# Kernel tuning notes

Hardware: AMD Instinct MI355X
Metric: run time of the kernel (lower is better)

Reference implementation:

```python
import jax, jax.numpy as jnp
import numpy as np

B, C_IN, L = 16, 64, 1024
HID, OUT, ORDER = 1024, 512, 4
EPS = 1e-5


def setup_inputs() -> dict:
    key = jax.random.key(0)
    ks = jax.random.split(key, 4)
    return {
        "x": jax.random.normal(ks[0], (B, C_IN, L), jnp.float32),
        "W_in": jax.random.normal(ks[1], (C_IN, HID), jnp.float32) / np.sqrt(C_IN).astype(np.float32),
        "b_in": jnp.zeros((HID,), jnp.float32),
        "coeffs1": jax.random.normal(ks[2], (HID, HID, ORDER), jnp.float32) * 0.01,
        "bias1": jnp.zeros((HID,), jnp.float32),
        "g1": jnp.ones((HID,), jnp.float32),
        "beta1": jnp.zeros((HID,), jnp.float32),
        "coeffs2": jax.random.normal(ks[3], (OUT, HID, ORDER), jnp.float32) * 0.01,
        "bias2": jnp.zeros((OUT,), jnp.float32),
        "g2": jnp.ones((OUT,), jnp.float32),
        "beta2": jnp.zeros((OUT,), jnp.float32),
    }


def _taylor_kan(x, coeffs, bias):
    # x: (B, L, C_in); coeffs: (out, C_in, order); y[b,l,o] = sum_i sum_c x^i * coeffs[o,c,i]
    # Expressed as order-wise GEMMs with a running power -- no (B,out,L,C) expand.
    order = coeffs.shape[-1]
    y = jnp.zeros(x.shape[:2] + (coeffs.shape[0],), x.dtype)
    xp = jnp.ones_like(x)  # x**0 (matches torch 0**0 == 1)
    for i in range(order):
        y = y + jnp.einsum('blc,oc->blo', xp, coeffs[:, :, i])
        if i + 1 < order:
            xp = xp * x
    return y + bias


def _layernorm(x, g, b):
    mu = jnp.mean(x, -1, keepdims=True)
    var = jnp.mean((x - mu) ** 2, -1, keepdims=True)
    return (x - mu) * jax.lax.rsqrt(var + EPS) * g + b


def reference(x, W_in, b_in, coeffs1, bias1, g1, beta1, coeffs2, bias2, g2, beta2):
    # x: (B, C_in, L) -> project channels to hidden: (B, L, HID)
    h = jnp.einsum('bcl,ch->blh', x, W_in) + b_in
    h = _taylor_kan(h, coeffs1, bias1)            # (B, L, HID)
    h = jax.nn.gelu(_layernorm(h, g1, beta1), approximate=False)
    h = _taylor_kan(h, coeffs2, bias2)            # (B, L, OUT)
    h = _layernorm(h, g2, beta2)
    return jnp.mean(h, axis=1)                    # adaptive avg pool over L -> (B, OUT)
```

## Files before the change

kernel.cpp:

```cpp
#include <hip/hip_runtime.h>
#include <math.h>

#define Bsz  16
#define CIN  64
#define LEN  1024
#define HIDN 1024
#define OUTN 512
#define MTOT (Bsz*LEN)
#define KTOT (3*HIDN)
#define KT1  (2*HIDN + CIN)
#define LCHUNKS 32
#define LROWS   (LEN/LCHUNKS)

typedef __attribute__((ext_vector_type(8))) short bf16x8;
typedef __attribute__((ext_vector_type(16))) float f32x16;

__device__ __forceinline__ unsigned short f2bf(float x) {
    union { float f; unsigned int u; } v; v.f = x;
    unsigned int r = v.u + 0x7fff + ((v.u >> 16) & 1);
    return (unsigned short)(r >> 16);
}
__device__ __forceinline__ float bf2f(unsigned short u) {
    union { unsigned int u; float f; } v; v.u = ((unsigned int)u) << 16;
    return v.f;
}
__device__ __forceinline__ void gload_lds16(const void* g, void* l) {
    __builtin_amdgcn_global_load_lds((const __attribute__((address_space(1))) void*)g,
                                     (__attribute__((address_space(3))) void*)l, 16, 0, 0);
}

__global__ __launch_bounds__(256) void prep_all(const float* __restrict__ coeffs1,
                                                const float* __restrict__ bias1,
                                                const float* __restrict__ coeffs2,
                                                const float* __restrict__ bias2,
                                                const float* __restrict__ x,
                                                const float* __restrict__ Win,
                                                unsigned short* __restrict__ W1T,
                                                float* __restrict__ b1e,
                                                unsigned short* __restrict__ W2T,
                                                float* __restrict__ b2e,
                                                unsigned short* __restrict__ xT,
                                                unsigned short* __restrict__ WinT) {
    __shared__ float sm[64 * 65];
    int bid = blockIdx.x, t = threadIdx.x;
    if (bid < 1024) {
        int o = bid;
        float s = 0.f;
        unsigned short* wrow = W1T + (size_t)o * KT1;
        for (int c = t; c < HIDN; c += 256) {
            float4 v = *(const float4*)(coeffs1 + ((size_t)o * HIDN + c) * 4);
            s += v.x;
            wrow[c]        = f2bf(v.z);
            wrow[HIDN + c] = f2bf(v.w);
        }
        for (int off = 32; off > 0; off >>= 1) s += __shfl_down(s, off, 64);
        if ((t & 63) == 0) sm[t >> 6] = s;
        __syncthreads();
        if (t == 0) b1e[o] = bias1[o] + sm[0] + sm[1] + sm[2] + sm[3];
    } else if (bid < 1536) {
        int o = bid - 1024;
        float s = 0.f;
        unsigned short* wrow = W2T + (size_t)o * KTOT;
        for (int c = t; c < HIDN; c += 256) {
            float4 v = *(const float4*)(coeffs2 + ((size_t)o * HIDN + c) * 4);
            s += v.x;
            wrow[c]            = f2bf(v.y);
            wrow[HIDN + c]     = f2bf(v.z);
            wrow[2 * HIDN + c] = f2bf(v.w);
        }
        for (int off = 32; off > 0; off >>= 1) s += __shfl_down(s, off, 64);
        if ((t & 63) == 0) sm[t >> 6] = s;
        __syncthreads();
        if (t == 0) b2e[o] = bias2[o] + sm[0] + sm[1] + sm[2] + sm[3];
    } else {
        const float* src; unsigned short* dstbase; size_t src_rstride;
        int c0;
        if (bid < 1792) {
            int tile = bid - 1536; int b = tile >> 4; c0 = (tile & 15) * 64;
            src = x + (size_t)b * CIN * LEN;  src_rstride = LEN;
            dstbase = xT + ((size_t)b * LEN + c0) * CIN;
        } else {
            int tile = bid - 1792; c0 = tile * 64;
            src = Win; src_rstride = HIDN;
            dstbase = WinT + (size_t)c0 * CIN;
        }
#pragma unroll
        for (int it = 0; it < 4; it++) {
            int idx = t + it * 256;
            int c = idx >> 4, q = idx & 15;
            float4 v = *(const float4*)(src + (size_t)c * src_rstride + c0 + q * 4);
            sm[c * 65 + q * 4 + 0] = v.x;
            sm[c * 65 + q * 4 + 1] = v.y;
            sm[c * 65 + q * 4 + 2] = v.z;
            sm[c * 65 + q * 4 + 3] = v.w;
        }
        __syncthreads();
        int ll = t >> 2, cg = (t & 3) * 16;
        unsigned short* dst = dstbase + (size_t)ll * CIN + cg;
#pragma unroll
        for (int j = 0; j < 4; j++) {
            int c = cg + j * 4;
            ushort4 w = { f2bf(sm[(c + 0) * 65 + ll]), f2bf(sm[(c + 1) * 65 + ll]),
                          f2bf(sm[(c + 2) * 65 + ll]), f2bf(sm[(c + 3) * 65 + ll]) };
            *(ushort4*)(dst + j * 4) = w;
        }
    }
}

__global__ __launch_bounds__(256) void wc1_kernel(const float* __restrict__ coeffs1,
                                                  const unsigned short* __restrict__ WinT,
                                                  const float* __restrict__ bin,
                                                  unsigned short* __restrict__ W1T,
                                                  float* __restrict__ b1e) {
    __shared__ float c1s[HIDN];
    __shared__ float part[4][64];
    __shared__ float pbred[4];
    int o = blockIdx.x, t = threadIdx.x, lane = t & 63, wave = t >> 6;
    for (int c = t; c < HIDN; c += 256)
        c1s[c] = coeffs1[((size_t)o * HIDN + c) * 4 + 1];
    __syncthreads();
    float acc = 0.f;
    int cbase = wave * 256;
    for (int c = cbase; c < cbase + 256; c++)
        acc += bf2f(WinT[c * CIN + lane]) * c1s[c];
    part[wave][lane] = acc;
    float pb = 0.f;
    for (int c = t; c < HIDN; c += 256) pb += bin[c] * c1s[c];
    for (int off = 32; off > 0; off >>= 1) pb += __shfl_down(pb, off, 64);
    if (lane == 0) pbred[wave] = pb;
    __syncthreads();
    if (t < 64) {
        float v = part[0][t] + part[1][t] + part[2][t] + part[3][t];
        W1T[(size_t)o * KT1 + 2 * HIDN + t] = f2bf(v);
    }
    if (t == 0) b1e[o] += pbred[0] + pbred[1] + pbred[2] + pbred[3];
}

__global__ __launch_bounds__(256) void proj_mfma(const unsigned short* __restrict__ xT,
                                                 const unsigned short* __restrict__ WinT,
                                                 const float* __restrict__ bin,
                                                 unsigned short* __restrict__ A1) {
    __shared__ unsigned short smem[2 * 128 * 64];
    unsigned short* As = smem;
    unsigned short* Bs = smem + 128 * 64;
    unsigned short* ht = smem;
    int t = threadIdx.x, lane = t & 63, wave = t >> 6;
    int m0 = blockIdx.x * 128, n0 = blockIdx.y * 128;
    int srow = lane >> 3, sgcc = (lane & 7) ^ srow;
    const unsigned short* Ab = xT + (size_t)m0 * CIN;
    const unsigned short* Bb = WinT + (size_t)n0 * CIN;

    f32x16 acc[2][2] = {};
    int wr = (wave >> 1) * 64, wc = (wave & 1) * 64;
    int row32 = lane & 31, half = lane >> 5;

#pragma unroll
    for (int j = 0; j < 4; j++) {
        int rgrp = wave * 32 + j * 8;
        gload_lds16(Ab + (size_t)(rgrp + srow) * CIN + sgcc * 8, As + rgrp * 64);
        gload_lds16(Bb + (size_t)(rgrp + srow) * CIN + sgcc * 8, Bs + rgrp * 64);
    }
    __syncthreads();
#pragma unroll
    for (int ks = 0; ks < 4; ks++) {
        int cidx = ks * 2 + half;
        bf16x8 af[2], bf[2];
#pragma unroll
        for (int mt = 0; mt < 2; mt++) {
            int r = wr + mt * 32 + row32;
            af[mt] = *(const bf16x8*)(As + r * 64 + ((cidx ^ (r & 7)) << 3));
        }
#pragma unroll
        for (int nt = 0; nt < 2; nt++) {
            int c = wc + nt * 32 + row32;
            bf[nt] = *(const bf16x8*)(Bs + c * 64 + ((cidx ^ (c & 7)) << 3));
        }
#pragma unroll
        for (int mt = 0; mt < 2; mt++)
#pragma unroll
            for (int nt = 0; nt < 2; nt++)
                acc[mt][nt] = __builtin_amdgcn_mfma_f32_32x32x16_bf16(af[mt], bf[nt], acc[mt][nt], 0, 0, 0);
    }
    __syncthreads();
#pragma unroll
    for (int nt = 0; nt < 2; nt++) {
        int ocl = wc + nt * 32 + row32;
        float bo = bin[n0 + ocl];
#pragma unroll
        for (int mt = 0; mt < 2; mt++) {
#pragma unroll
            for (int reg = 0; reg < 16; reg++) {
                int rl = wr + mt * 32 + (reg & 3) + 8 * (reg >> 2) + 4 * half;
                ht[rl * 128 + ocl] = f2bf(acc[mt][nt][reg] + bo);
            }
        }
    }
    __syncthreads();
#pragma unroll
    for (int p = 0; p < 8; p++) {
        int r = p * 16 + (t >> 4);
        int c = (t & 15) * 8;
        bf16x8 hv = *(const bf16x8*)(ht + r * 128 + c);
        bf16x8 h2v, h3v;
#pragma unroll
        for (int j = 0; j < 8; j++) {
            float f = bf2f((unsigned short)hv[j]);
            float f2 = f * f;
            h2v[j] = (short)f2bf(f2);
            h3v[j] = (short)f2bf(f2 * f);
        }
        unsigned short* d = A1 + (size_t)(m0 + r) * KT1 + n0 + c;
        *(bf16x8*)(d)        = h2v;
        *(bf16x8*)(d + HIDN) = h3v;
    }
    if (n0 == 0) {
#pragma unroll
        for (int it = 0; it < 4; it++) {
            int idx = t + it * 256;
            int r = idx >> 3, cc = (idx & 7) * 8;
            bf16x8 v = *(const bf16x8*)(xT + (size_t)(m0 + r) * CIN + cc);
            *(bf16x8*)(A1 + (size_t)(m0 + r) * KT1 + 2 * HIDN + cc) = v;
        }
    }
}

template<int N, int KT, bool BF16OUT>
__global__ __launch_bounds__(256) void mfma_gemm(const unsigned short* __restrict__ A,
                                                 const unsigned short* __restrict__ BT,
                                                 const float* __restrict__ beff,
                                                 void* __restrict__ Yv) {
    __shared__ unsigned short As[128 * 64];
    __shared__ unsigned short Bs[128 * 64];
    int t = threadIdx.x;
    int lane = t & 63, wave = t >> 6;
    int m0 = blockIdx.x * 128, n0 = blockIdx.y * 128;
    const unsigned short* Ab = A + (size_t)m0 * KT;
    const unsigned short* Bb = BT + (size_t)n0 * KT;

    int srow = lane >> 3;
    int sgcc = (lane & 7) ^ srow;

    f32x16 acc[2][2] = {};
    int wr = (wave >> 1) * 64;
    int wc = (wave & 1) * 64;
    int row32 = lane & 31, half = lane >> 5;

    for (int k0 = 0; k0 < KT; k0 += 64) {
#pragma unroll
        for (int j = 0; j < 4; j++) {
            int rgrp = wave * 32 + j * 8;
            gload_lds16(Ab + ((size_t)(rgrp + srow) * KT + k0 + sgcc * 8), As + rgrp * 64);
            gload_lds16(Bb + ((size_t)(rgrp + srow) * KT + k0 + sgcc * 8), Bs + rgrp * 64);
        }
        __syncthreads();
#pragma unroll
        for (int ks = 0; ks < 4; ks++) {
            int cidx = ks * 2 + half;
            bf16x8 af[2], bf[2];
#pragma unroll
            for (int mt = 0; mt < 2; mt++) {
                int r = wr + mt * 32 + row32;
                af[mt] = *(const bf16x8*)(As + r * 64 + ((cidx ^ (r & 7)) << 3));
            }
#pragma unroll
            for (int nt = 0; nt < 2; nt++) {
                int c = wc + nt * 32 + row32;
                bf[nt] = *(const bf16x8*)(Bs + c * 64 + ((cidx ^ (c & 7)) << 3));
            }
#pragma unroll
            for (int mt = 0; mt < 2; mt++)
#pragma unroll
                for (int nt = 0; nt < 2; nt++)
                    acc[mt][nt] = __builtin_amdgcn_mfma_f32_32x32x16_bf16(af[mt], bf[nt], acc[mt][nt], 0, 0, 0);
        }
        __syncthreads();
    }
#pragma unroll
    for (int nt = 0; nt < 2; nt++) {
        int oc = n0 + wc + nt * 32 + row32;
        float bo = beff[oc];
#pragma unroll
        for (int mt = 0; mt < 2; mt++) {
#pragma unroll
            for (int reg = 0; reg < 16; reg++) {
                int rl = (reg & 3) + 8 * (reg >> 2) + 4 * half;
                int mr = m0 + wr + mt * 32 + rl;
                float v = acc[mt][nt][reg] + bo;
                if (BF16OUT) ((unsigned short*)Yv)[(size_t)mr * N + oc] = f2bf(v);
                else         ((float*)Yv)[(size_t)mr * N + oc] = v;
            }
        }
    }
}

__global__ __launch_bounds__(256) void ln_gelu(const unsigned short* __restrict__ y1,
                                               const float* __restrict__ g,
                                               const float* __restrict__ be,
                                               unsigned short* __restrict__ Gpow) {
    __shared__ float2 red[2][2];
    int t = threadIdx.x;
    int rhalf = t >> 7, l = t & 127, wid = (t >> 6) & 1;
    int m = blockIdx.x * 2 + rhalf;
    bf16x8 u = *(const bf16x8*)(y1 + (size_t)m * HIDN + l * 8);
    float v[8];
    float s = 0.f, ss = 0.f;
#pragma unroll
    for (int j = 0; j < 8; j++) {
        v[j] = bf2f((unsigned short)u[j]);
        s += v[j]; ss += v[j] * v[j];
    }
    for (int off = 32; off > 0; off >>= 1) {
        s  += __shfl_down(s, off, 64);
        ss += __shfl_down(ss, off, 64);
    }
    if ((t & 63) == 0) red[rhalf][wid] = make_float2(s, ss);
    __syncthreads();
    float sT  = red[rhalf][0].x + red[rhalf][1].x;
    float ssT = red[rhalf][0].y + red[rhalf][1].y;
    float mu = sT * (1.f / HIDN);
    float var = ssT * (1.f / HIDN) - mu * mu;
    float rs = rsqrtf(var + 1e-5f);
    float4 gA = *(const float4*)(g + l * 8),  gB = *(const float4*)(g + l * 8 + 4);
    float4 bA = *(const float4*)(be + l * 8), bB = *(const float4*)(be + l * 8 + 4);
    float gv[8] = { gA.x, gA.y, gA.z, gA.w, gB.x, gB.y, gB.z, gB.w };
    float bv[8] = { bA.x, bA.y, bA.z, bA.w, bB.x, bB.y, bB.z, bB.w };
    bf16x8 p1, p2, p3;
#pragma unroll
    for (int j = 0; j < 8; j++) {
        float xn = (v[j] - mu) * rs * gv[j] + bv[j];
        float gl = xn * 0.5f * (1.f + erff(xn * 0.70710678118654752f));
        float g2 = gl * gl;
        p1[j] = (short)f2bf(gl);
        p2[j] = (short)f2bf(g2);
        p3[j] = (short)f2bf(g2 * gl);
    }
    unsigned short* dst = Gpow + (size_t)m * KTOT + l * 8;
    *(bf16x8*)(dst)            = p1;
    *(bf16x8*)(dst + HIDN)     = p2;
    *(bf16x8*)(dst + 2 * HIDN) = p3;
}

__global__ __launch_bounds__(256) void ln_pool_partial(const unsigned short* __restrict__ y2,
                                                       const float* __restrict__ g,
                                                       const float* __restrict__ be,
                                                       float* __restrict__ partial) {
    __shared__ float part[4][OUTN];
    int t = threadIdx.x, lane = t & 63, wave = t >> 6;
    int b = blockIdx.x, chunk = blockIdx.y;
    int mbase = b * LEN + chunk * LROWS;

    float4 gA = *(const float4*)(g + 8 * lane),  gB = *(const float4*)(g + 8 * lane + 4);
    float4 bA = *(const float4*)(be + 8 * lane), bB = *(const float4*)(be + 8 * lane + 4);
    float gv[8] = { gA.x, gA.y, gA.z, gA.w, gB.x, gB.y, gB.z, gB.w };
    float bv[8] = { bA.x, bA.y, bA.z, bA.w, bB.x, bB.y, bB.z, bB.w };

    float acc[8] = {0.f, 0.f, 0.f, 0.f, 0.f, 0.f, 0.f, 0.f};
    for (int rr = wave; rr < LROWS; rr += 4) {
        bf16x8 u = *(const bf16x8*)(y2 + (size_t)(mbase + rr) * OUTN + 8 * lane);
        float v[8];
        float s = 0.f, ss = 0.f;
#pragma unroll
        for (int j = 0; j < 8; j++) {
            v[j] = bf2f((unsigned short)u[j]);
            s += v[j]; ss += v[j] * v[j];
        }
        for (int off = 32; off > 0; off >>= 1) {
            s  += __shfl_down(s, off, 64);
            ss += __shfl_down(ss, off, 64);
        }
        s  = __shfl(s, 0, 64);
        ss = __shfl(ss, 0, 64);
        float mu = s * (1.f / OUTN);
        float var = ss * (1.f / OUTN) - mu * mu;
        float rs = rsqrtf(var + 1e-5f);
#pragma unroll
        for (int j = 0; j < 8; j++)
            acc[j] += (v[j] - mu) * rs * gv[j] + bv[j];
    }
    *(float4*)(&part[wave][8 * lane])     = *(float4*)(&acc[0]);
    *(float4*)(&part[wave][8 * lane + 4]) = *(float4*)(&acc[4]);
    __syncthreads();
    float p0 = part[0][2*t] + part[1][2*t] + part[2][2*t] + part[3][2*t];
    float p1 = part[0][2*t+1] + part[1][2*t+1] + part[2][2*t+1] + part[3][2*t+1];
    float* dst = partial + ((size_t)b * LCHUNKS + chunk) * OUTN;
    *(float2*)(dst + 2 * t) = make_float2(p0, p1);
}

__global__ __launch_bounds__(256) void pool_reduce(const float* __restrict__ partial,
                                                   float* __restrict__ out) {
    int b = blockIdx.x, t = threadIdx.x;
    const float* src = partial + (size_t)b * LCHUNKS * OUTN;
    float s0 = 0.f, s1 = 0.f;
    for (int c = 0; c < LCHUNKS; c++) {
        float2 v = *(const float2*)(src + (size_t)c * OUTN + 2 * t);
        s0 += v.x; s1 += v.y;
    }
    *(float2*)(out + (size_t)b * OUTN + 2 * t) = make_float2(s0 * (1.f / LEN), s1 * (1.f / LEN));
}

extern "C" void kernel_launch(void* const* d_in, const int* in_sizes, int n_in,
                              void* d_out, int out_size, void* d_ws, size_t ws_size,
                              hipStream_t stream) {
    const float* x       = (const float*)d_in[0];
    const float* Win     = (const float*)d_in[1];
    const float* bin     = (const float*)d_in[2];
    const float* coeffs1 = (const float*)d_in[3];
    const float* bias1   = (const float*)d_in[4];
    const float* g1      = (const float*)d_in[5];
    const float* beta1   = (const float*)d_in[6];
    const float* coeffs2 = (const float*)d_in[7];
    const float* bias2   = (const float*)d_in[8];
    const float* g2      = (const float*)d_in[9];
    const float* beta2   = (const float*)d_in[10];
    float* out = (float*)d_out;

    char* ws = (char*)d_ws;
    unsigned short* A1   = (unsigned short*)ws;
    unsigned short* Gpow = (unsigned short*)ws;
    char* p1 = ws + (size_t)MTOT * KTOT * 2;
    unsigned short* y1   = (unsigned short*)p1;
    unsigned short* y2   = (unsigned short*)p1;
    char* p2 = p1 + (size_t)MTOT * HIDN * 2;
    unsigned short* W1T  = (unsigned short*)p2;
    char* p3 = p2 + (size_t)HIDN * KT1 * 2;
    unsigned short* W2T  = (unsigned short*)p3;
    char* p4 = p3 + (size_t)OUTN * KTOT * 2;
    float* b1e = (float*)p4;
    float* b2e = (float*)(p4 + HIDN * sizeof(float));
    char* p5 = p4 + (HIDN + OUTN) * sizeof(float);
    unsigned short* xT   = (unsigned short*)p5;
    char* p6 = p5 + (size_t)MTOT * CIN * 2;
    unsigned short* WinT = (unsigned short*)p6;
    float* partial = (float*)W1T;

    prep_all<<<1808, 256, 0, stream>>>(coeffs1, bias1, coeffs2, bias2, x, Win,
                                       W1T, b1e, W2T, b2e, xT, WinT);
    wc1_kernel<<<HIDN, 256, 0, stream>>>(coeffs1, WinT, bin, W1T, b1e);
    proj_mfma<<<dim3(MTOT / 128, HIDN / 128), 256, 0, stream>>>(xT, WinT, bin, A1);
    mfma_gemm<HIDN, KT1, true><<<dim3(MTOT / 128, HIDN / 128), 256, 0, stream>>>(A1, W1T, b1e, y1);
    ln_gelu<<<MTOT / 2, 256, 0, stream>>>(y1, g1, beta1, Gpow);
    mfma_gemm<OUTN, KTOT, true><<<dim3(MTOT / 128, OUTN / 128), 256, 0, stream>>>(Gpow, W2T, b2e, y2);
    ln_pool_partial<<<dim3(Bsz, LCHUNKS), 256, 0, stream>>>(y2, g2, beta2, partial);
    pool_reduce<<<Bsz, 256, 0, stream>>>(partial, out);
}
```

Before: 288.9 us.

## Compute GELU powers inside second GEMM and fold wc1 into projection kernel

ln_gelu now writes only the GELU activation (1024 columns) instead of three power planes. The second KAN GEMM computes the squared and cubed fragments in registers from the loaded tile and issues three MFMAs per step against three slices of the weights, which cuts the write and read traffic of the 3x-wide activation matrix. The separate wc1_kernel is merged into the tail of proj_mfma: each of the 1024 blocks handles one output row and uses an atomicAdd on the bias, which removes one launch. The price is extra conversion arithmetic in the GEMM inner loop, 64 KB of shared memory per block that may lower occupancy, and a serial tail appended to the projection blocks.

```diff
diff --git a/kernel.cpp b/kernel.cpp
--- a/kernel.cpp
+++ b/kernel.cpp
@@ -1,4 +1,5 @@
 #include <hip/hip_runtime.h>
+#include <hip/hip_bf16.h>
 #include <math.h>
 
 #define Bsz  16
@@ -27,6 +28,18 @@
 __device__ __forceinline__ void gload_lds16(const void* g, void* l) {
     __builtin_amdgcn_global_load_lds((const __attribute__((address_space(1))) void*)g,
                                      (__attribute__((address_space(3))) void*)l, 16, 0, 0);
+}
+__device__ __forceinline__ void powfrags(const bf16x8& a, bf16x8& a2, bf16x8& a3) {
+#pragma unroll
+    for (int j = 0; j < 4; j++) {
+        float f0 = bf2f((unsigned short)a[2 * j]);
+        float f1 = bf2f((unsigned short)a[2 * j + 1]);
+        float s0 = f0 * f0, s1 = f1 * f1;
+        __hip_bfloat162 p2 = __float22bfloat162_rn(float2{ s0, s1 });
+        __hip_bfloat162 p3 = __float22bfloat162_rn(float2{ s0 * f0, s1 * f1 });
+        ((unsigned int*)&a2)[j] = *(unsigned int*)&p2;
+        ((unsigned int*)&a3)[j] = *(unsigned int*)&p3;
+    }
 }
 
 __global__ __launch_bounds__(256) void prep_all(const float* __restrict__ coeffs1,
@@ -107,39 +120,13 @@
     }
 }
 
-__global__ __launch_bounds__(256) void wc1_kernel(const float* __restrict__ coeffs1,
-                                                  const unsigned short* __restrict__ WinT,
-                                                  const float* __restrict__ bin,
-                                                  unsigned short* __restrict__ W1T,
-                                                  float* __restrict__ b1e) {
-    __shared__ float c1s[HIDN];
-    __shared__ float part[4][64];
-    __shared__ float pbred[4];
-    int o = blockIdx.x, t = threadIdx.x, lane = t & 63, wave = t >> 6;
-    for (int c = t; c < HIDN; c += 256)
-        c1s[c] = coeffs1[((size_t)o * HIDN + c) * 4 + 1];
-    __syncthreads();
-    float acc = 0.f;
-    int cbase = wave * 256;
-    for (int c = cbase; c < cbase + 256; c++)
-        acc += bf2f(WinT[c * CIN + lane]) * c1s[c];
-    part[wave][lane] = acc;
-    float pb = 0.f;
-    for (int c = t; c < HIDN; c += 256) pb += bin[c] * c1s[c];
-    for (int off = 32; off > 0; off >>= 1) pb += __shfl_down(pb, off, 64);
-    if (lane == 0) pbred[wave] = pb;
-    __syncthreads();
-    if (t < 64) {
-        float v = part[0][t] + part[1][t] + part[2][t] + part[3][t];
-        W1T[(size_t)o * KT1 + 2 * HIDN + t] = f2bf(v);
-    }
-    if (t == 0) b1e[o] += pbred[0] + pbred[1] + pbred[2] + pbred[3];
-}
-
 __global__ __launch_bounds__(256) void proj_mfma(const unsigned short* __restrict__ xT,
                                                  const unsigned short* __restrict__ WinT,
                                                  const float* __restrict__ bin,
-                                                 unsigned short* __restrict__ A1) {
+                                                 unsigned short* __restrict__ A1,
+                                                 const float* __restrict__ coeffs1,
+                                                 unsigned short* __restrict__ W1T,
+                                                 float* __restrict__ b1e) {
     __shared__ unsigned short smem[2 * 128 * 64];
     unsigned short* As = smem;
     unsigned short* Bs = smem + 128 * 64;
@@ -222,6 +209,31 @@
             *(bf16x8*)(A1 + (size_t)(m0 + r) * KT1 + 2 * HIDN + cc) = v;
         }
     }
+    int o = blockIdx.x * 8 + blockIdx.y;
+    __syncthreads();
+    float* c1s   = (float*)smem;
+    float* part  = (float*)smem + 1024;
+    float* pbred = part + 256;
+    for (int c = t; c < HIDN; c += 256) {
+        float4 v = *(const float4*)(coeffs1 + ((size_t)o * HIDN + c) * 4);
+        c1s[c] = v.y;
+    }
+    __syncthreads();
+    float a1 = 0.f;
+    int cbase = wave * 256;
+    for (int c = cbase; c < cbase + 256; c++)
+        a1 += bf2f(WinT[c * CIN + lane]) * c1s[c];
+    part[wave * 64 + lane] = a1;
+    float pb = 0.f;
+    for (int c = t; c < HIDN; c += 256) pb += bin[c] * c1s[c];
+    for (int off = 32; off > 0; off >>= 1) pb += __shfl_down(pb, off, 64);
+    if (lane == 0) pbred[wave] = pb;
+    __syncthreads();
+    if (t < 64) {
+        float v = part[t] + part[64 + t] + part[128 + t] + part[192 + t];
+        W1T[(size_t)o * KT1 + 2 * HIDN + t] = f2bf(v);
+    }
+    if (t == 0) atomicAdd(&b1e[o], pbred[0] + pbred[1] + pbred[2] + pbred[3]);
 }
 
 template<int N, int KT, bool BF16OUT>
@@ -296,7 +308,7 @@
 __global__ __launch_bounds__(256) void ln_gelu(const unsigned short* __restrict__ y1,
                                                const float* __restrict__ g,
                                                const float* __restrict__ be,
-                                               unsigned short* __restrict__ Gpow) {
+                                               unsigned short* __restrict__ Gonly) {
     __shared__ float2 red[2][2];
     int t = threadIdx.x;
     int rhalf = t >> 7, l = t & 127, wid = (t >> 6) & 1;
@@ -324,20 +336,85 @@
     float4 bA = *(const float4*)(be + l * 8), bB = *(const float4*)(be + l * 8 + 4);
     float gv[8] = { gA.x, gA.y, gA.z, gA.w, gB.x, gB.y, gB.z, gB.w };
     float bv[8] = { bA.x, bA.y, bA.z, bA.w, bB.x, bB.y, bB.z, bB.w };
-    bf16x8 p1, p2, p3;
+    bf16x8 p1;
 #pragma unroll
     for (int j = 0; j < 8; j++) {
         float xn = (v[j] - mu) * rs * gv[j] + bv[j];
         float gl = xn * 0.5f * (1.f + erff(xn * 0.70710678118654752f));
-        float g2 = gl * gl;
         p1[j] = (short)f2bf(gl);
-        p2[j] = (short)f2bf(g2);
-        p3[j] = (short)f2bf(g2 * gl);
-    }
-    unsigned short* dst = Gpow + (size_t)m * KTOT + l * 8;
-    *(bf16x8*)(dst)            = p1;
-    *(bf16x8*)(dst + HIDN)     = p2;
-    *(bf16x8*)(dst + 2 * HIDN) = p3;
+    }
+    *(bf16x8*)(Gonly + (size_t)m * HIDN + l * 8) = p1;
+}
+
+__global__ __launch_bounds__(256) void kan2_gemm(const unsigned short* __restrict__ G,
+                                                 const unsigned short* __restrict__ W2T,
+                                                 const float* __restrict__ beff,
+                                                 unsigned short* __restrict__ Y) {
+    __shared__ unsigned short smem[128 * 64 * 4];
+    unsigned short* As = smem;
+    unsigned short* Bs = smem + 128 * 64;
+    int t = threadIdx.x, lane = t & 63, wave = t >> 6;
+    int m0 = blockIdx.x * 128, n0 = blockIdx.y * 128;
+    int srow = lane >> 3, sgcc = (lane & 7) ^ srow;
+    const unsigned short* Ab = G + (size_t)m0 * HIDN;
+    const unsigned short* Bb = W2T + (size_t)n0 * KTOT;
+
+    f32x16 acc[2][2] = {};
+    int wr = (wave >> 1) * 64, wc = (wave & 1) * 64;
+    int row32 = lane & 31, half = lane >> 5;
+
+    for (int c0 = 0; c0 < HIDN; c0 += 64) {
+#pragma unroll
+        for (int j = 0; j < 4; j++) {
+            int rgrp = wave * 32 + j * 8;
+            gload_lds16(Ab + ((size_t)(rgrp + srow) * HIDN + c0 + sgcc * 8), As + rgrp * 64);
+#pragma unroll
+            for (int p = 0; p < 3; p++)
+                gload_lds16(Bb + ((size_t)(rgrp + srow) * KTOT + p * HIDN + c0 + sgcc * 8),
+                            Bs + p * 128 * 64 + rgrp * 64);
+        }
+        __syncthreads();
+#pragma unroll
+        for (int ks = 0; ks < 4; ks++) {
+            int cidx = ks * 2 + half;
+            bf16x8 af[2], af2[2], af3[2];
+#pragma unroll
+            for (int mt = 0; mt < 2; mt++) {
+                int r = wr + mt * 32 + row32;
+                af[mt] = *(const bf16x8*)(As + r * 64 + ((cidx ^ (r & 7)) << 3));
+                powfrags(af[mt], af2[mt], af3[mt]);
+            }
+#pragma unroll
+            for (int nt = 0; nt < 2; nt++) {
+                int c = wc + nt * 32 + row32;
+                int boff = c * 64 + ((cidx ^ (c & 7)) << 3);
+                bf16x8 b1 = *(const bf16x8*)(Bs + boff);
+                bf16x8 b2 = *(const bf16x8*)(Bs + 128 * 64 + boff);
+                bf16x8 b3 = *(const bf16x8*)(Bs + 2 * 128 * 64 + boff);
+#pragma unroll
+                for (int mt = 0; mt < 2; mt++) {
+                    acc[mt][nt] = __builtin_amdgcn_mfma_f32_32x32x16_bf16(af[mt],  b1, acc[mt][nt], 0, 0, 0);
+                    acc[mt][nt] = __builtin_amdgcn_mfma_f32_32x32x16_bf16(af2[mt], b2, acc[mt][nt], 0, 0, 0);
+                    acc[mt][nt] = __builtin_amdgcn_mfma_f32_32x32x16_bf16(af3[mt], b3, acc[mt][nt], 0, 0, 0);
+                }
+            }
+        }
+        __syncthreads();
+    }
+#pragma unroll
+    for (int nt = 0; nt < 2; nt++) {
+        int oc = n0 + wc + nt * 32 + row32;
+        float bo = beff[oc];
+#pragma unroll
+        for (int mt = 0; mt < 2; mt++) {
+#pragma unroll
+            for (int reg = 0; reg < 16; reg++) {
+                int rl = (reg & 3) + 8 * (reg >> 2) + 4 * half;
+                int mr = m0 + wr + mt * 32 + rl;
+                Y[(size_t)mr * OUTN + oc] = f2bf(acc[mt][nt][reg] + bo);
+            }
+        }
+    }
 }
 
 __global__ __launch_bounds__(256) void ln_pool_partial(const unsigned short* __restrict__ y2,
@@ -415,8 +492,8 @@
     float* out = (float*)d_out;
 
     char* ws = (char*)d_ws;
-    unsigned short* A1   = (unsigned short*)ws;
-    unsigned short* Gpow = (unsigned short*)ws;
+    unsigned short* A1    = (unsigned short*)ws;
+    unsigned short* Gonly = (unsigned short*)ws;
     char* p1 = ws + (size_t)MTOT * KTOT * 2;
     unsigned short* y1   = (unsigned short*)p1;
     unsigned short* y2   = (unsigned short*)p1;
@@ -435,11 +512,11 @@
 
     prep_all<<<1808, 256, 0, stream>>>(coeffs1, bias1, coeffs2, bias2, x, Win,
                                        W1T, b1e, W2T, b2e, xT, WinT);
-    wc1_kernel<<<HIDN, 256, 0, stream>>>(coeffs1, WinT, bin, W1T, b1e);
-    proj_mfma<<<dim3(MTOT / 128, HIDN / 128), 256, 0, stream>>>(xT, WinT, bin, A1);
+    proj_mfma<<<dim3(MTOT / 128, HIDN / 128), 256, 0, stream>>>(xT, WinT, bin, A1,
+                                                                coeffs1, W1T, b1e);
     mfma_gemm<HIDN, KT1, true><<<dim3(MTOT / 128, HIDN / 128), 256, 0, stream>>>(A1, W1T, b1e, y1);
-    ln_gelu<<<MTOT / 2, 256, 0, stream>>>(y1, g1, beta1, Gpow);
-    mfma_gemm<OUTN, KTOT, true><<<dim3(MTOT / 128, OUTN / 128), 256, 0, stream>>>(Gpow, W2T, b2e, y2);
+    ln_gelu<<<MTOT / 2, 256, 0, stream>>>(y1, g1, beta1, Gonly);
+    kan2_gemm<<<dim3(MTOT / 128, OUTN / 128), 256, 0, stream>>>(Gonly, W2T, b2e, y2);
     ln_pool_partial<<<dim3(Bsz, LCHUNKS), 256, 0, stream>>>(y2, g2, beta2, partial);
     pool_reduce<<<Bsz, 256, 0, stream>>>(partial, out);
 }
```

Measured after the change: 286.9 us. Within noise of the previous version (-0.7%).
